# Optimization experiments

Measured on AMD Instinct MI355X. Metric: run time of the kernel, lower is better.

## Reference

```python
import jax, jax.numpy as jnp
import numpy as np

N_HEADS = 16
D_EMBD = 1024
D_HEAD = D_EMBD // N_HEADS  # 64


def setup_inputs() -> dict:
    key = jax.random.key(0)
    k0, k1, k2, k3, k4 = jax.random.split(key, 5)
    s = 1.0 / np.sqrt(D_EMBD)
    return {
        "x": jax.random.normal(k0, (4, 2048, D_EMBD), dtype=jnp.float32),
        "w_in": jax.random.normal(k1, (D_EMBD, 3 * D_EMBD), dtype=jnp.float32) * s,
        "b_in": jax.random.normal(k2, (3 * D_EMBD,), dtype=jnp.float32) * 0.02,
        "w_out": jax.random.normal(k3, (D_EMBD, D_EMBD), dtype=jnp.float32) * s,
        "b_out": jax.random.normal(k4, (D_EMBD,), dtype=jnp.float32) * 0.02,
    }


def reference(x, w_in, b_in, w_out, b_out):
    B, S, D = x.shape
    # fused QKV projection; torch .chunk(3) order in source is k, q, v
    kqv = x @ w_in + b_in                      # [B, S, 3D]
    k, q, v = jnp.split(kqv, 3, axis=-1)
    # split heads: [B, S, D] -> [B, H, S, Dh]
    def heads(t):
        return t.reshape(B, S, N_HEADS, D_HEAD).transpose(0, 2, 1, 3)
    q, k, v = heads(q), heads(k), heads(v)
    # attention scores, explicit O(S^2) matrix (naive, unmasked path)
    scores = jnp.einsum("bhsd,bhtd->bhst", q, k) / jnp.sqrt(
        jnp.asarray(D_HEAD, dtype=x.dtype)
    )
    probs = jax.nn.softmax(scores, axis=-1)    # [B, H, S, S]
    out = jnp.einsum("bhst,bhtd->bhsd", probs, v)
    out = out.transpose(0, 2, 1, 3).reshape(B, S, D)
    return out @ w_out + b_out
```

## Files before the change

kernel.cpp:

```cpp
#include <hip/hip_runtime.h>

typedef unsigned short u16;
typedef __attribute__((ext_vector_type(8))) short bf16x8;
typedef __attribute__((ext_vector_type(4))) float f32x4;

#define MFMA(a, b, c) __builtin_amdgcn_mfma_f32_16x16x32_bf16(a, b, c, 0, 0, 0)

#if defined(__has_builtin)
#if __has_builtin(__builtin_amdgcn_exp2f)
#define EXP2(x) __builtin_amdgcn_exp2f(x)
#endif
#endif
#ifndef EXP2
#define EXP2(x) exp2f(x)
#endif

#define ASYNC16(g, l)                                                      \
  __builtin_amdgcn_global_load_lds(                                        \
      (const __attribute__((address_space(1))) void*)(g),                  \
      (__attribute__((address_space(3))) void*)(l), 16, 0, 0)

__device__ __forceinline__ u16 f2bf(float x) {
  union { float f; unsigned u; } v; v.f = x;
  unsigned r = (v.u + 0x7fffu + ((v.u >> 16) & 1u)) >> 16;
  return (u16)r;
}

__device__ __forceinline__ unsigned pack_bf2(float a, float b) {
  unsigned ua = __float_as_uint(a) + 0x8000u;
  unsigned ub = __float_as_uint(b) + 0x8000u;
  return __builtin_amdgcn_perm(ub, ua, 0x07060302u);
}

__device__ __forceinline__ bf16x8 exp_pack8(const f32x4 a, const f32x4 b) {
  union { unsigned u[4]; bf16x8 v; } r;
  r.u[0] = pack_bf2(EXP2(a[0]), EXP2(a[1]));
  r.u[1] = pack_bf2(EXP2(a[2]), EXP2(a[3]));
  r.u[2] = pack_bf2(EXP2(b[0]), EXP2(b[1]));
  r.u[3] = pack_bf2(EXP2(b[2]), EXP2(b[3]));
  return r.v;
}

__global__ void transpose_to_bf16(const float* __restrict__ in, u16* __restrict__ out,
                                  int R, int C) {
  __shared__ float tile[32][33];
  int c0 = blockIdx.x * 32, r0 = blockIdx.y * 32;
  int tx = threadIdx.x, ty = threadIdx.y;
#pragma unroll
  for (int i = 0; i < 32; i += 8)
    tile[ty + i][tx] = in[(size_t)(r0 + ty + i) * C + c0 + tx];
  __syncthreads();
#pragma unroll
  for (int i = 0; i < 32; i += 8)
    out[(size_t)(c0 + ty + i) * R + r0 + tx] = f2bf(tile[tx][ty + i]);
}

__global__ void f32_to_bf16_vec(const float4* __restrict__ in, uint2* __restrict__ out) {
  int idx = blockIdx.x * 256 + threadIdx.x;
  float4 v = in[idx];
  out[idx] = make_uint2(pack_bf2(v.x, v.y), pack_bf2(v.z, v.w));
}

#define BM 128
#define BN 128
#define BK 64

template <int OUT_F32, int NBX>
__global__ __launch_bounds__(256, 2) void gemm_bt(const u16* __restrict__ A,
                                                  const u16* __restrict__ Bt,
                                                  const float* __restrict__ bias,
                                                  void* __restrict__ Cout,
                                                  int M, int N, int K, int ldc,
                                                  int sc_lo, int sc_hi, float qs) {
  __shared__ __align__(16) u16 As[BM * BK];
  __shared__ __align__(16) u16 Bs[BN * BK];
  int id = blockIdx.x;
  int cpx = gridDim.x >> 3;
  int swz = (id & 7) * cpx + (id >> 3);
  int bn = (swz % NBX) * BN, bm = (swz / NBX) * BM;
  int tid = threadIdx.x;
  int wave = tid >> 6, lane = tid & 63;
  int quad = lane >> 4, l16 = lane & 15;
  int wm = (wave >> 1) * 64, wn = (wave & 1) * 64;

  f32x4 acc[4][4] = {};

  int lrow = lane >> 3, lcol = (lane & 7) * 8;
  const u16* gA = A + (size_t)(bm + wave * 8 + lrow) * K + lcol;
  const u16* gB = Bt + (size_t)(bn + wave * 8 + lrow) * K + lcol;
  u16* lA = &As[wave * 8 * BK];
  u16* lB = &Bs[wave * 8 * BK];

  for (int k0 = 0; k0 < K; k0 += BK) {
#pragma unroll
    for (int p = 0; p < 4; ++p) {
      ASYNC16(gA + (size_t)p * 32 * K, lA + p * 32 * BK);
      ASYNC16(gB + (size_t)p * 32 * K, lB + p * 32 * BK);
    }
    gA += BK;
    gB += BK;
    __syncthreads();
#pragma unroll
    for (int kk = 0; kk < BK; kk += 32) {
      bf16x8 af[4], bfr[4];
#pragma unroll
      for (int i = 0; i < 4; ++i)
        af[i] = *(const bf16x8*)&As[(wm + 16 * i + l16) * BK + kk + quad * 8];
#pragma unroll
      for (int j = 0; j < 4; ++j)
        bfr[j] = *(const bf16x8*)&Bs[(wn + 16 * j + l16) * BK + kk + quad * 8];
#pragma unroll
      for (int i = 0; i < 4; ++i)
#pragma unroll
        for (int j = 0; j < 4; ++j)
          acc[i][j] = MFMA(af[i], bfr[j], acc[i][j]);
    }
    __syncthreads();
  }

#pragma unroll
  for (int i = 0; i < 4; ++i) {
#pragma unroll
    for (int j = 0; j < 4; ++j) {
      int gn = bn + wn + 16 * j + l16;
      float bv = bias[gn];
      float sc = (gn >= sc_lo && gn < sc_hi) ? qs : 1.0f;
#pragma unroll
      for (int r = 0; r < 4; ++r) {
        int gm = bm + wm + 16 * i + quad * 4 + r;
        float v = (acc[i][j][r] + bv) * sc;
        if (OUT_F32)
          ((float*)Cout)[(size_t)gm * ldc + gn] = v;
        else
          ((u16*)Cout)[(size_t)gm * ldc + gn] = f2bf(v);
      }
    }
  }
}

#define SEQ 2048
#define ROWS3 3072

__global__ void v_transpose(const u16* __restrict__ kqv, u16* __restrict__ vt) {
  int bh = blockIdx.y;
  int b = bh >> 4, h = bh & 15;
  int t0 = blockIdx.x * 64;
  int tid = threadIdx.x;
  __shared__ u16 tile[64][72];
  int r = tid >> 3, c = (tid & 7) * 8;
#pragma unroll
  for (int p = 0; p < 2; ++p)
    *(uint4*)&tile[p * 32 + r][c] =
        *(const uint4*)&kqv[(size_t)b * SEQ * ROWS3 + (size_t)(t0 + p * 32 + r) * ROWS3 +
                            2048 + h * 64 + c];
  __syncthreads();
#pragma unroll
  for (int p = 0; p < 2; ++p) {
    int d = p * 32 + r;
    u16 tmp[8];
#pragma unroll
    for (int i = 0; i < 8; ++i) {
      int pos = c + i;
      int k = 16 * (2 * (pos >> 5) + ((pos >> 2) & 1)) + ((pos >> 3) & 3) * 4 + (pos & 3);
      tmp[i] = tile[k][d];
    }
    *(uint4*)&vt[(size_t)bh * 64 * SEQ + (size_t)d * SEQ + t0 + c] = *(uint4*)tmp;
  }
}

__global__ __launch_bounds__(256, 4) void attn_kernel(const u16* __restrict__ kqv,
                                                      const u16* __restrict__ vt,
                                                      u16* __restrict__ out) {
  int g = blockIdx.x;
  int bh = g & 63, qtile = g >> 6;
  int b = bh >> 4, h = bh & 15;
  int tid = threadIdx.x, wave = tid >> 6, lane = tid & 63;
  int quad = lane >> 4, l16 = lane & 15;

  __shared__ __align__(16) u16 Ks[2][64 * 64];
  __shared__ __align__(16) u16 Vts[2][64 * 64];

  const u16* base = kqv + (size_t)b * SEQ * ROWS3;
  int hcol = h * 64;
  const u16* vbase = vt + (size_t)bh * 64 * SEQ;

  bf16x8 qf[2][2];
#pragma unroll
  for (int t = 0; t < 2; ++t) {
    int s = qtile * 128 + wave * 32 + t * 16 + l16;
    const u16* qrow = base + (size_t)s * ROWS3 + 1024 + hcol;
    qf[t][0] = *(const bf16x8*)(qrow + quad * 8);
    qf[t][1] = *(const bf16x8*)(qrow + 32 + quad * 8);
  }

  bf16x8 ones;
#pragma unroll
  for (int i = 0; i < 8; ++i) ones[i] = (short)0x3F80;

  f32x4 o[2][4] = {};
  f32x4 ol[2] = {};
  const f32x4 zf = {};

  int prow = lane & 7;
  int pchk = (lane >> 3) * 8;

  int rb2 = (l16 >> 3) * 512;
  int r8 = (l16 & 7) * 8;

  const u16* kg = base + hcol + (size_t)(wave * 16 + prow) * ROWS3 + pchk;
  const u16* vg = vbase + (size_t)(wave * 16 + prow) * SEQ + pchk;

  ASYNC16(kg, &Ks[0][wave * 16 * 64]);
  ASYNC16(kg + (size_t)8 * ROWS3, &Ks[0][(wave * 16 + 8) * 64]);
  ASYNC16(vg, &Vts[0][wave * 16 * 64]);
  ASYNC16(vg + (size_t)8 * SEQ, &Vts[0][(wave * 16 + 8) * 64]);

  int cur = 0;

  for (int t0 = 0; t0 < SEQ; t0 += 64) {
    __syncthreads();

    if (t0 + 64 < SEQ) {
      kg += (size_t)64 * ROWS3;
      vg += 64;
      ASYNC16(kg, &Ks[cur ^ 1][wave * 16 * 64]);
      ASYNC16(kg + (size_t)8 * ROWS3, &Ks[cur ^ 1][(wave * 16 + 8) * 64]);
      ASYNC16(vg, &Vts[cur ^ 1][wave * 16 * 64]);
      ASYNC16(vg + (size_t)8 * SEQ, &Vts[cur ^ 1][(wave * 16 + 8) * 64]);
    }

    const u16* ks = &Ks[cur][0];
    const u16* vs = &Vts[cur][0];

    __builtin_amdgcn_s_setprio(1);

    f32x4 s0[4], s1[4];
#pragma unroll
    for (int j = 0; j < 4; ++j) {
      bf16x8 k0 = *(const bf16x8*)&ks[j * 1024 + rb2 + quad * 64 + r8];
      bf16x8 k1 = *(const bf16x8*)&ks[j * 1024 + rb2 + 256 + quad * 64 + r8];
      s0[j] = MFMA(k0, qf[0][0], zf);
      s0[j] = MFMA(k1, qf[0][1], s0[j]);
      s1[j] = MFMA(k0, qf[1][0], zf);
      s1[j] = MFMA(k1, qf[1][1], s1[j]);
    }

    bf16x8 pa[2][2];
    pa[0][0] = exp_pack8(s0[0], s0[1]);
    pa[0][1] = exp_pack8(s0[2], s0[3]);
    pa[1][0] = exp_pack8(s1[0], s1[1]);
    pa[1][1] = exp_pack8(s1[2], s1[3]);

#pragma unroll
    for (int d = 0; d < 4; ++d) {
      bf16x8 v0 = *(const bf16x8*)&vs[d * 1024 + rb2 + quad * 64 + r8];
      bf16x8 v1 = *(const bf16x8*)&vs[d * 1024 + rb2 + 256 + quad * 64 + r8];
      o[0][d] = MFMA(pa[0][0], v0, o[0][d]);
      o[0][d] = MFMA(pa[0][1], v1, o[0][d]);
      o[1][d] = MFMA(pa[1][0], v0, o[1][d]);
      o[1][d] = MFMA(pa[1][1], v1, o[1][d]);
    }
    ol[0] = MFMA(pa[0][0], ones, ol[0]);
    ol[0] = MFMA(pa[0][1], ones, ol[0]);
    ol[1] = MFMA(pa[1][0], ones, ol[1]);
    ol[1] = MFMA(pa[1][1], ones, ol[1]);

    __builtin_amdgcn_s_setprio(0);

    cur ^= 1;
  }

#pragma unroll
  for (int t = 0; t < 2; ++t)
#pragma unroll
    for (int r = 0; r < 4; ++r) {
      float inv = 1.0f / ol[t][r];
      int s = qtile * 128 + wave * 32 + t * 16 + quad * 4 + r;
      u16* orow = out + (size_t)(b * SEQ + s) * 1024 + hcol;
#pragma unroll
      for (int d = 0; d < 4; ++d) orow[16 * d + l16] = f2bf(o[t][d][r] * inv);
    }
}

extern "C" void kernel_launch(void* const* d_in, const int* in_sizes, int n_in,
                              void* d_out, int out_size, void* d_ws, size_t ws_size,
                              hipStream_t stream) {
  const float* x     = (const float*)d_in[0];
  const float* w_in  = (const float*)d_in[1];
  const float* b_in  = (const float*)d_in[2];
  const float* w_out = (const float*)d_in[3];
  const float* b_out = (const float*)d_in[4];
  float* outp = (float*)d_out;

  char* p = (char*)d_ws;
  u16* wT_in  = (u16*)p; p += (size_t)3072 * 1024 * 2;
  u16* wT_out = (u16*)p; p += (size_t)1024 * 1024 * 2;
  u16* xb     = (u16*)p; p += (size_t)8192 * 1024 * 2;
  u16* kqv    = (u16*)p; p += (size_t)8192 * 3072 * 2;
  u16* attn   = (u16*)p;
  u16* vtbuf  = xb;

  transpose_to_bf16<<<dim3(3072 / 32, 1024 / 32), dim3(32, 8), 0, stream>>>(w_in, wT_in, 1024, 3072);
  transpose_to_bf16<<<dim3(1024 / 32, 1024 / 32), dim3(32, 8), 0, stream>>>(w_out, wT_out, 1024, 1024);
  f32_to_bf16_vec<<<dim3(8192), dim3(256), 0, stream>>>((const float4*)x, (uint2*)xb);

  const float QSCALE = 0.125f * 1.44269504088896f;
  gemm_bt<0, 3072 / BN><<<dim3((3072 / BN) * (8192 / BM)), 256, 0, stream>>>(
      xb, wT_in, b_in, (void*)kqv, 8192, 3072, 1024, 3072, 1024, 2048, QSCALE);

  v_transpose<<<dim3(SEQ / 64, 64), 256, 0, stream>>>(kqv, vtbuf);

  attn_kernel<<<dim3(1024), 256, 0, stream>>>(kqv, vtbuf, attn);

  gemm_bt<1, 1024 / BN><<<dim3((1024 / BN) * (8192 / BM)), 256, 0, stream>>>(
      attn, wT_out, b_out, (void*)outp, 8192, 1024, 1024, 1024, 0, 0, 1.0f);
}
```

Measured before the change: 279.3 us.

## Add 256x256-tile double-buffered bf16 GEMM for the QKV projection

Adds a new GEMM kernel with 256x256 output tiles, 512 threads and 64-wide K steps. Operands are loaded into double-buffered LDS through async global-to-LDS copies, MFMA work runs at raised wave priority, and block IDs are swizzled. The QKV projection now uses this kernel instead of the smaller-tile gemm_bt, aiming for more operand reuse per LDS load and overlap of loads with compute. The cost is 128KB of LDS per block, so only one block fits per CU, and the 384-block grid leaves an uneven last wave.

```diff
diff --git a/kernel.cpp b/kernel.cpp
--- a/kernel.cpp
+++ b/kernel.cpp
@@ -138,6 +138,106 @@
   }
 }
 
+#define GN256 256
+#define GK256 64
+
+template <int OUT_F32, int NBX>
+__global__ __launch_bounds__(512, 2) void gemm256(const u16* __restrict__ A,
+                                                  const u16* __restrict__ Bt,
+                                                  const float* __restrict__ bias,
+                                                  void* __restrict__ Cout,
+                                                  int K, int ldc,
+                                                  int sc_lo, int sc_hi, float qs) {
+  __shared__ __align__(16) u16 As[2][256 * 64];
+  __shared__ __align__(16) u16 Bs[2][256 * 64];
+
+  int id = blockIdx.x;
+  int cpx = gridDim.x >> 3;
+  int swz = (id & 7) * cpx + (id >> 3);
+  int bn = (swz % NBX) * 256, bm = (swz / NBX) * 256;
+
+  int tid = threadIdx.x;
+  int w = tid >> 6, lane = tid & 63;
+  int quad = lane >> 4, l16 = lane & 15;
+  int wm2 = w >> 2, wn4 = w & 3;
+
+  f32x4 acc[8][4] = {};
+
+  const u16* gAbase = A + (size_t)(bm + w * 8 + (lane & 7)) * K + (lane >> 3) * 8;
+  const u16* gBbase = Bt + (size_t)(bn + w * 8 + (lane & 7)) * K + (lane >> 3) * 8;
+
+  int a_base = (wm2 * 16 + (l16 >> 3)) * 512 + quad * 64 + (l16 & 7) * 8;
+  int b_base = (wn4 * 8 + (l16 >> 3)) * 512 + quad * 64 + (l16 & 7) * 8;
+
+  int NKT = K >> 6;
+
+#pragma unroll
+  for (int qa = 0; qa < 4; ++qa) {
+    ASYNC16(gAbase + (size_t)(qa * 64) * K, &As[0][w * 512 + qa * 4096]);
+    ASYNC16(gBbase + (size_t)(qa * 64) * K, &Bs[0][w * 512 + qa * 4096]);
+  }
+
+  int cur = 0;
+  for (int kt = 0; kt < NKT; ++kt) {
+    __syncthreads();
+
+    if (kt + 1 < NKT) {
+      int k0 = (kt + 1) * GK256;
+#pragma unroll
+      for (int qa = 0; qa < 4; ++qa) {
+        ASYNC16(gAbase + (size_t)(qa * 64) * K + k0, &As[cur ^ 1][w * 512 + qa * 4096]);
+        ASYNC16(gBbase + (size_t)(qa * 64) * K + k0, &Bs[cur ^ 1][w * 512 + qa * 4096]);
+      }
+    }
+
+    const u16* ab = &As[cur][a_base];
+    const u16* bb = &Bs[cur][b_base];
+
+    __builtin_amdgcn_s_setprio(1);
+#pragma unroll
+    for (int kk = 0; kk < 2; ++kk) {
+      bf16x8 bfr[4];
+#pragma unroll
+      for (int j = 0; j < 4; ++j)
+        bfr[j] = *(const bf16x8*)&bb[j * 1024 + kk * 256];
+#pragma unroll
+      for (int i = 0; i < 8; ++i) {
+        bf16x8 af = *(const bf16x8*)&ab[i * 1024 + kk * 256];
+#pragma unroll
+        for (int j = 0; j < 4; ++j)
+          acc[i][j] = MFMA(af, bfr[j], acc[i][j]);
+      }
+    }
+    __builtin_amdgcn_s_setprio(0);
+    cur ^= 1;
+  }
+
+  float bvs[4], scj[4];
+#pragma unroll
+  for (int j = 0; j < 4; ++j) {
+    int gn = bn + wn4 * 64 + 16 * j + l16;
+    bvs[j] = bias[gn];
+    scj[j] = (gn >= sc_lo && gn < sc_hi) ? qs : 1.0f;
+  }
+#pragma unroll
+  for (int i = 0; i < 8; ++i) {
+#pragma unroll
+    for (int r = 0; r < 4; ++r) {
+      int gm = bm + wm2 * 128 + 16 * i + quad * 4 + r;
+      size_t rbase = (size_t)gm * ldc + bn + wn4 * 64 + l16;
+      if (OUT_F32) {
+        float* rp = (float*)Cout + rbase;
+#pragma unroll
+        for (int j = 0; j < 4; ++j) rp[16 * j] = (acc[i][j][r] + bvs[j]) * scj[j];
+      } else {
+        u16* rp = (u16*)Cout + rbase;
+#pragma unroll
+        for (int j = 0; j < 4; ++j) rp[16 * j] = f2bf((acc[i][j][r] + bvs[j]) * scj[j]);
+      }
+    }
+  }
+}
+
 #define SEQ 2048
 #define ROWS3 3072
 
@@ -305,8 +405,8 @@
   f32_to_bf16_vec<<<dim3(8192), dim3(256), 0, stream>>>((const float4*)x, (uint2*)xb);
 
   const float QSCALE = 0.125f * 1.44269504088896f;
-  gemm_bt<0, 3072 / BN><<<dim3((3072 / BN) * (8192 / BM)), 256, 0, stream>>>(
-      xb, wT_in, b_in, (void*)kqv, 8192, 3072, 1024, 3072, 1024, 2048, QSCALE);
+  gemm256<0, 3072 / 256><<<dim3(384), 512, 0, stream>>>(
+      xb, wT_in, b_in, (void*)kqv, 1024, 3072, 1024, 2048, QSCALE);
 
   v_transpose<<<dim3(SEQ / 64, 64), 256, 0, stream>>>(kqv, vtbuf);
 
```

New measurement: 314.8 us. 1.13x slower.

## Software-pipeline QK^T of next tile with PV of current tile in attention

Applied to the files above, without the earlier changes.

Restructures the attention main loop so the QK^T MFMAs and exp for tile t+1 are issued in the same iteration as the PV MFMAs for tile t. This lets exp/VALU work overlap with matrix work. To make that safe, V gets a triple buffer while K stays double-buffered, and a prologue and epilogue handle the first and last tiles. LDS use grows by 8 KB per block, which could lower occupancy at launch_bounds(256,4), and the extra live P registers add register pressure.

```diff
diff --git a/kernel.cpp b/kernel.cpp
--- a/kernel.cpp
+++ b/kernel.cpp
@@ -178,7 +178,7 @@
   int quad = lane >> 4, l16 = lane & 15;
 
   __shared__ __align__(16) u16 Ks[2][64 * 64];
-  __shared__ __align__(16) u16 Vts[2][64 * 64];
+  __shared__ __align__(16) u16 Vts[3][64 * 64];
 
   const u16* base = kqv + (size_t)b * SEQ * ROWS3;
   int hcol = h * 64;
@@ -210,30 +210,30 @@
   const u16* kg = base + hcol + (size_t)(wave * 16 + prow) * ROWS3 + pchk;
   const u16* vg = vbase + (size_t)(wave * 16 + prow) * SEQ + pchk;
 
-  ASYNC16(kg, &Ks[0][wave * 16 * 64]);
-  ASYNC16(kg + (size_t)8 * ROWS3, &Ks[0][(wave * 16 + 8) * 64]);
-  ASYNC16(vg, &Vts[0][wave * 16 * 64]);
-  ASYNC16(vg + (size_t)8 * SEQ, &Vts[0][(wave * 16 + 8) * 64]);
-
-  int cur = 0;
-
-  for (int t0 = 0; t0 < SEQ; t0 += 64) {
-    __syncthreads();
-
-    if (t0 + 64 < SEQ) {
-      kg += (size_t)64 * ROWS3;
-      vg += 64;
-      ASYNC16(kg, &Ks[cur ^ 1][wave * 16 * 64]);
-      ASYNC16(kg + (size_t)8 * ROWS3, &Ks[cur ^ 1][(wave * 16 + 8) * 64]);
-      ASYNC16(vg, &Vts[cur ^ 1][wave * 16 * 64]);
-      ASYNC16(vg + (size_t)8 * SEQ, &Vts[cur ^ 1][(wave * 16 + 8) * 64]);
-    }
-
-    const u16* ks = &Ks[cur][0];
-    const u16* vs = &Vts[cur][0];
-
-    __builtin_amdgcn_s_setprio(1);
-
+#define STAGE_K(bi)                                      \
+  do {                                                   \
+    ASYNC16(kg, &Ks[bi][wave * 16 * 64]);                \
+    ASYNC16(kg + (size_t)8 * ROWS3, &Ks[bi][(wave * 16 + 8) * 64]); \
+    kg += (size_t)64 * ROWS3;                            \
+  } while (0)
+#define STAGE_V(bi)                                      \
+  do {                                                   \
+    ASYNC16(vg, &Vts[bi][wave * 16 * 64]);               \
+    ASYNC16(vg + (size_t)8 * SEQ, &Vts[bi][(wave * 16 + 8) * 64]); \
+    vg += 64;                                            \
+  } while (0)
+
+  const int NT = SEQ / 64;
+
+  STAGE_K(0);
+  STAGE_V(0);
+  __syncthreads();
+  STAGE_K(1);
+  STAGE_V(1);
+
+  bf16x8 pa00, pa01, pa10, pa11;
+  {
+    const u16* ks = &Ks[0][0];
     f32x4 s0[4], s1[4];
 #pragma unroll
     for (int j = 0; j < 4; ++j) {
@@ -244,30 +244,83 @@
       s1[j] = MFMA(k0, qf[1][0], zf);
       s1[j] = MFMA(k1, qf[1][1], s1[j]);
     }
-
-    bf16x8 pa[2][2];
-    pa[0][0] = exp_pack8(s0[0], s0[1]);
-    pa[0][1] = exp_pack8(s0[2], s0[3]);
-    pa[1][0] = exp_pack8(s1[0], s1[1]);
-    pa[1][1] = exp_pack8(s1[2], s1[3]);
+    pa00 = exp_pack8(s0[0], s0[1]);
+    pa01 = exp_pack8(s0[2], s0[3]);
+    pa10 = exp_pack8(s1[0], s1[1]);
+    pa11 = exp_pack8(s1[2], s1[3]);
+  }
+
+  int v_rd = 0;
+  int v_st = 2;
+
+  for (int t = 0; t < NT - 1; ++t) {
+    __syncthreads();
+
+    if (t + 2 < NT) {
+      STAGE_K(t & 1);
+      STAGE_V(v_st);
+    }
+
+    const u16* ks = &Ks[(t + 1) & 1][0];
+    const u16* vs = &Vts[v_rd][0];
+
+    __builtin_amdgcn_s_setprio(1);
+
+    f32x4 s0[4], s1[4];
+#pragma unroll
+    for (int j = 0; j < 4; ++j) {
+      bf16x8 k0 = *(const bf16x8*)&ks[j * 1024 + rb2 + quad * 64 + r8];
+      bf16x8 k1 = *(const bf16x8*)&ks[j * 1024 + rb2 + 256 + quad * 64 + r8];
+      s0[j] = MFMA(k0, qf[0][0], zf);
+      s0[j] = MFMA(k1, qf[0][1], s0[j]);
+      s1[j] = MFMA(k0, qf[1][0], zf);
+      s1[j] = MFMA(k1, qf[1][1], s1[j]);
+    }
+
+    bf16x8 pn00 = exp_pack8(s0[0], s0[1]);
+    bf16x8 pn01 = exp_pack8(s0[2], s0[3]);
+    bf16x8 pn10 = exp_pack8(s1[0], s1[1]);
+    bf16x8 pn11 = exp_pack8(s1[2], s1[3]);
 
 #pragma unroll
     for (int d = 0; d < 4; ++d) {
       bf16x8 v0 = *(const bf16x8*)&vs[d * 1024 + rb2 + quad * 64 + r8];
       bf16x8 v1 = *(const bf16x8*)&vs[d * 1024 + rb2 + 256 + quad * 64 + r8];
-      o[0][d] = MFMA(pa[0][0], v0, o[0][d]);
-      o[0][d] = MFMA(pa[0][1], v1, o[0][d]);
-      o[1][d] = MFMA(pa[1][0], v0, o[1][d]);
-      o[1][d] = MFMA(pa[1][1], v1, o[1][d]);
-    }
-    ol[0] = MFMA(pa[0][0], ones, ol[0]);
-    ol[0] = MFMA(pa[0][1], ones, ol[0]);
-    ol[1] = MFMA(pa[1][0], ones, ol[1]);
-    ol[1] = MFMA(pa[1][1], ones, ol[1]);
+      o[0][d] = MFMA(pa00, v0, o[0][d]);
+      o[0][d] = MFMA(pa01, v1, o[0][d]);
+      o[1][d] = MFMA(pa10, v0, o[1][d]);
+      o[1][d] = MFMA(pa11, v1, o[1][d]);
+    }
+    ol[0] = MFMA(pa00, ones, ol[0]);
+    ol[0] = MFMA(pa01, ones, ol[0]);
+    ol[1] = MFMA(pa10, ones, ol[1]);
+    ol[1] = MFMA(pa11, ones, ol[1]);
 
     __builtin_amdgcn_s_setprio(0);
 
-    cur ^= 1;
+    pa00 = pn00; pa01 = pn01; pa10 = pn10; pa11 = pn11;
+    v_rd = (v_rd == 2) ? 0 : v_rd + 1;
+    v_st = (v_st == 2) ? 0 : v_st + 1;
+  }
+
+  __syncthreads();
+  {
+    const u16* vs = &Vts[v_rd][0];
+    __builtin_amdgcn_s_setprio(1);
+#pragma unroll
+    for (int d = 0; d < 4; ++d) {
+      bf16x8 v0 = *(const bf16x8*)&vs[d * 1024 + rb2 + quad * 64 + r8];
+      bf16x8 v1 = *(const bf16x8*)&vs[d * 1024 + rb2 + 256 + quad * 64 + r8];
+      o[0][d] = MFMA(pa00, v0, o[0][d]);
+      o[0][d] = MFMA(pa01, v1, o[0][d]);
+      o[1][d] = MFMA(pa10, v0, o[1][d]);
+      o[1][d] = MFMA(pa11, v1, o[1][d]);
+    }
+    ol[0] = MFMA(pa00, ones, ol[0]);
+    ol[0] = MFMA(pa01, ones, ol[0]);
+    ol[1] = MFMA(pa10, ones, ol[1]);
+    ol[1] = MFMA(pa11, ones, ol[1]);
+    __builtin_amdgcn_s_setprio(0);
   }
 
 #pragma unroll
@@ -280,6 +333,8 @@
 #pragma unroll
       for (int d = 0; d < 4; ++d) orow[16 * d + l16] = f2bf(o[t][d][r] * inv);
     }
+#undef STAGE_K
+#undef STAGE_V
 }
 
 extern "C" void kernel_launch(void* const* d_in, const int* in_sizes, int n_in,
```

Result: no change. 279.6 us (+0.1%).

## Switch attention kernel to 32x32x16 MFMA tiles with matching V-transpose permutation

Applied to the files above, without the earlier changes.

Replaces the 16x16x32 bf16 MFMA instructions in the attention inner loop with 32x32x16 MFMAs, so each wave computes its 32 query rows as one 32-row tile. The LDS fragment addressing, the exp/pack of scores into A-operand fragments, the row-sum accumulation and the output write-back are all reworked for the 32x32 register layout. The V-transpose kernel's key permutation is changed so the P fragment layout lines up with V. The aim is fewer MFMA issues and LDS reads per tile, at the cost of larger accumulator vectors and more register pressure.

```diff
diff --git a/kernel.cpp b/kernel.cpp
--- a/kernel.cpp
+++ b/kernel.cpp
@@ -3,8 +3,10 @@
 typedef unsigned short u16;
 typedef __attribute__((ext_vector_type(8))) short bf16x8;
 typedef __attribute__((ext_vector_type(4))) float f32x4;
+typedef __attribute__((ext_vector_type(16))) float f32x16;
 
 #define MFMA(a, b, c) __builtin_amdgcn_mfma_f32_16x16x32_bf16(a, b, c, 0, 0, 0)
+#define MFMA32(a, b, c) __builtin_amdgcn_mfma_f32_32x32x16_bf16(a, b, c, 0, 0, 0)
 
 #if defined(__has_builtin)
 #if __has_builtin(__builtin_amdgcn_exp2f)
@@ -32,14 +34,15 @@
   return __builtin_amdgcn_perm(ub, ua, 0x07060302u);
 }
 
-__device__ __forceinline__ bf16x8 exp_pack8(const f32x4 a, const f32x4 b) {
-  union { unsigned u[4]; bf16x8 v; } r;
-  r.u[0] = pack_bf2(EXP2(a[0]), EXP2(a[1]));
-  r.u[1] = pack_bf2(EXP2(a[2]), EXP2(a[3]));
-  r.u[2] = pack_bf2(EXP2(b[0]), EXP2(b[1]));
-  r.u[3] = pack_bf2(EXP2(b[2]), EXP2(b[3]));
-  return r.v;
-}
+#define EXP_PACK8(s, B)                                         \
+  ({                                                            \
+    union { unsigned u[4]; bf16x8 v; } r_;                      \
+    r_.u[0] = pack_bf2(EXP2((s)[(B) + 0]), EXP2((s)[(B) + 1])); \
+    r_.u[1] = pack_bf2(EXP2((s)[(B) + 2]), EXP2((s)[(B) + 3])); \
+    r_.u[2] = pack_bf2(EXP2((s)[(B) + 4]), EXP2((s)[(B) + 5])); \
+    r_.u[3] = pack_bf2(EXP2((s)[(B) + 6]), EXP2((s)[(B) + 7])); \
+    r_.v;                                                       \
+  })
 
 __global__ void transpose_to_bf16(const float* __restrict__ in, u16* __restrict__ out,
                                   int R, int C) {
@@ -161,7 +164,7 @@
 #pragma unroll
     for (int i = 0; i < 8; ++i) {
       int pos = c + i;
-      int k = 16 * (2 * (pos >> 5) + ((pos >> 2) & 1)) + ((pos >> 3) & 3) * 4 + (pos & 3);
+      int k = (pos & ~12) | ((pos & 8) >> 1) | ((pos & 4) << 1);
       tmp[i] = tile[k][d];
     }
     *(uint4*)&vt[(size_t)bh * 64 * SEQ + (size_t)d * SEQ + t0 + c] = *(uint4*)tmp;
@@ -175,7 +178,7 @@
   int bh = g & 63, qtile = g >> 6;
   int b = bh >> 4, h = bh & 15;
   int tid = threadIdx.x, wave = tid >> 6, lane = tid & 63;
-  int quad = lane >> 4, l16 = lane & 15;
+  int l32 = lane & 31, half = lane >> 5;
 
   __shared__ __align__(16) u16 Ks[2][64 * 64];
   __shared__ __align__(16) u16 Vts[2][64 * 64];
@@ -184,28 +187,25 @@
   int hcol = h * 64;
   const u16* vbase = vt + (size_t)bh * 64 * SEQ;
 
-  bf16x8 qf[2][2];
-#pragma unroll
-  for (int t = 0; t < 2; ++t) {
-    int s = qtile * 128 + wave * 32 + t * 16 + l16;
-    const u16* qrow = base + (size_t)s * ROWS3 + 1024 + hcol;
-    qf[t][0] = *(const bf16x8*)(qrow + quad * 8);
-    qf[t][1] = *(const bf16x8*)(qrow + 32 + quad * 8);
+  int qbase = qtile * 128 + wave * 32;
+  bf16x8 qf[4];
+  {
+    const u16* qrow = base + (size_t)(qbase + l32) * ROWS3 + 1024 + hcol;
+#pragma unroll
+    for (int ds = 0; ds < 4; ++ds) qf[ds] = *(const bf16x8*)(qrow + ds * 16 + half * 8);
   }
 
   bf16x8 ones;
 #pragma unroll
   for (int i = 0; i < 8; ++i) ones[i] = (short)0x3F80;
 
-  f32x4 o[2][4] = {};
-  f32x4 ol[2] = {};
-  const f32x4 zf = {};
+  f32x16 o0 = {}, o1 = {}, ol = {};
+  const f32x16 z16 = {};
 
   int prow = lane & 7;
   int pchk = (lane >> 3) * 8;
 
-  int rb2 = (l16 >> 3) * 512;
-  int r8 = (l16 & 7) * 8;
+  int fb = (l32 >> 3) * 512 + half * 64 + (l32 & 7) * 8;
 
   const u16* kg = base + hcol + (size_t)(wave * 16 + prow) * ROWS3 + pchk;
   const u16* vg = vbase + (size_t)(wave * 16 + prow) * SEQ + pchk;
@@ -234,36 +234,40 @@
 
     __builtin_amdgcn_s_setprio(1);
 
-    f32x4 s0[4], s1[4];
-#pragma unroll
-    for (int j = 0; j < 4; ++j) {
-      bf16x8 k0 = *(const bf16x8*)&ks[j * 1024 + rb2 + quad * 64 + r8];
-      bf16x8 k1 = *(const bf16x8*)&ks[j * 1024 + rb2 + 256 + quad * 64 + r8];
-      s0[j] = MFMA(k0, qf[0][0], zf);
-      s0[j] = MFMA(k1, qf[0][1], s0[j]);
-      s1[j] = MFMA(k0, qf[1][0], zf);
-      s1[j] = MFMA(k1, qf[1][1], s1[j]);
-    }
-
-    bf16x8 pa[2][2];
-    pa[0][0] = exp_pack8(s0[0], s0[1]);
-    pa[0][1] = exp_pack8(s0[2], s0[3]);
-    pa[1][0] = exp_pack8(s1[0], s1[1]);
-    pa[1][1] = exp_pack8(s1[2], s1[3]);
-
-#pragma unroll
-    for (int d = 0; d < 4; ++d) {
-      bf16x8 v0 = *(const bf16x8*)&vs[d * 1024 + rb2 + quad * 64 + r8];
-      bf16x8 v1 = *(const bf16x8*)&vs[d * 1024 + rb2 + 256 + quad * 64 + r8];
-      o[0][d] = MFMA(pa[0][0], v0, o[0][d]);
-      o[0][d] = MFMA(pa[0][1], v1, o[0][d]);
-      o[1][d] = MFMA(pa[1][0], v0, o[1][d]);
-      o[1][d] = MFMA(pa[1][1], v1, o[1][d]);
-    }
-    ol[0] = MFMA(pa[0][0], ones, ol[0]);
-    ol[0] = MFMA(pa[0][1], ones, ol[0]);
-    ol[1] = MFMA(pa[1][0], ones, ol[1]);
-    ol[1] = MFMA(pa[1][1], ones, ol[1]);
+    f32x16 s0, s1;
+    {
+      bf16x8 kf = *(const bf16x8*)&ks[fb];
+      s0 = MFMA32(kf, qf[0], z16);
+#pragma unroll
+      for (int ds = 1; ds < 4; ++ds) {
+        bf16x8 kf2 = *(const bf16x8*)&ks[fb + ds * 128];
+        s0 = MFMA32(kf2, qf[ds], s0);
+      }
+    }
+    {
+      bf16x8 kf = *(const bf16x8*)&ks[2048 + fb];
+      s1 = MFMA32(kf, qf[0], z16);
+#pragma unroll
+      for (int ds = 1; ds < 4; ++ds) {
+        bf16x8 kf2 = *(const bf16x8*)&ks[2048 + fb + ds * 128];
+        s1 = MFMA32(kf2, qf[ds], s1);
+      }
+    }
+
+    bf16x8 pa[4];
+    pa[0] = EXP_PACK8(s0, 0);
+    pa[1] = EXP_PACK8(s0, 8);
+    pa[2] = EXP_PACK8(s1, 0);
+    pa[3] = EXP_PACK8(s1, 8);
+
+#pragma unroll
+    for (int m = 0; m < 4; ++m) {
+      bf16x8 v0 = *(const bf16x8*)&vs[fb + m * 128];
+      bf16x8 v1 = *(const bf16x8*)&vs[2048 + fb + m * 128];
+      o0 = MFMA32(pa[m], v0, o0);
+      o1 = MFMA32(pa[m], v1, o1);
+      ol = MFMA32(pa[m], ones, ol);
+    }
 
     __builtin_amdgcn_s_setprio(0);
 
@@ -271,15 +275,13 @@
   }
 
 #pragma unroll
-  for (int t = 0; t < 2; ++t)
-#pragma unroll
-    for (int r = 0; r < 4; ++r) {
-      float inv = 1.0f / ol[t][r];
-      int s = qtile * 128 + wave * 32 + t * 16 + quad * 4 + r;
-      u16* orow = out + (size_t)(b * SEQ + s) * 1024 + hcol;
-#pragma unroll
-      for (int d = 0; d < 4; ++d) orow[16 * d + l16] = f2bf(o[t][d][r] * inv);
-    }
+  for (int p = 0; p < 16; ++p) {
+    float inv = 1.0f / ol[p];
+    int q = (p & 3) + 8 * (p >> 2) + 4 * half;
+    u16* orow = out + (size_t)(b * SEQ + qbase + q) * 1024 + hcol + l32;
+    orow[0] = f2bf(o0[p] * inv);
+    orow[32] = f2bf(o1[p] * inv);
+  }
 }
 
 extern "C" void kernel_launch(void* const* d_in, const int* in_sizes, int n_in,
```

Result: slower. 286.4 us (+2.5%).
